# Performance work log

Hardware: AMD Instinct MI355X
Metric: run time of the kernel (lower is better)

## Reference

```python
import jax, jax.numpy as jnp
import numpy as np

B, T, N, D, K = 8, 64, 512, 64, 8
d = D // K  # per-head dim
NEG = -(2.0 ** 15) + 1.0  # -32767, as in source


def setup_inputs() -> dict:
    key = jax.random.key(0)
    ks = jax.random.split(key, 12)
    s = 0.05
    inp = {
        "x": jax.random.normal(ks[0], (B, T, N, D), dtype=jnp.float32),
        "ste": jax.random.normal(ks[1], (B, T, N, D), dtype=jnp.float32),
        "Wq": jax.random.normal(ks[2], (2 * D, D), dtype=jnp.float32) * s,
        "bq": jnp.zeros((D,), dtype=jnp.float32),
        "Wk": jax.random.normal(ks[3], (2 * D, D), dtype=jnp.float32) * s,
        "bk": jnp.zeros((D,), dtype=jnp.float32),
        "Wv": jax.random.normal(ks[4], (2 * D, D), dtype=jnp.float32) * s,
        "bv": jnp.zeros((D,), dtype=jnp.float32),
        "W1": jax.random.normal(ks[5], (D, D), dtype=jnp.float32) * s,
        "b1": jnp.zeros((D,), dtype=jnp.float32),
        "W2": jax.random.normal(ks[6], (D, D), dtype=jnp.float32) * s,
        "b2": jnp.zeros((D,), dtype=jnp.float32),
    }
    return inp


def reference(x, ste, Wq, bq, Wk, bk, Wv, bv, W1, b1, W2, b2):
    h = jnp.concatenate([x, ste], axis=-1)  # (B,T,N,2D)
    q = jax.nn.relu(jnp.einsum("btnf,fd->btnd", h, Wq) + bq)
    k = jax.nn.relu(jnp.einsum("btnf,fd->btnd", h, Wk) + bk)
    v = jax.nn.relu(jnp.einsum("btnf,fd->btnd", h, Wv) + bv)
    # split D into K heads of size d (torch split/cat over batch == head axis)
    q = q.reshape(B, T, N, K, d)
    k = k.reshape(B, T, N, K, d)
    v = v.reshape(B, T, N, K, d)
    scores = jnp.einsum("btnkd,bsnkd->bnkts", q, k) / jnp.sqrt(jnp.float32(d))
    causal = jnp.tril(jnp.ones((T, T), dtype=bool))  # (T,T)
    scores = jnp.where(causal, scores, jnp.float32(NEG))
    attn = jax.nn.softmax(scores, axis=-1)  # (B,N,K,T,T)
    out = jnp.einsum("bnkts,bsnkd->btnkd", attn, v).reshape(B, T, N, D)
    out = jax.nn.relu(jnp.einsum("btnd,de->btne", out, W1) + b1)
    out = jnp.einsum("btnd,de->btne", out, W2) + b2
    return out
```

## Files before the change

kernel.cpp:

```cpp
#include <hip/hip_runtime.h>


#define Bb 8
#define Tt 64
#define Nn 512
#define Dd 64

typedef unsigned short u16;
typedef unsigned int u32;
typedef __bf16 bf16x8 __attribute__((ext_vector_type(8)));
typedef float f32x4 __attribute__((ext_vector_type(4)));
typedef short s16x8 __attribute__((ext_vector_type(8)));

#define HS 136
#define QS 68

#define QSCALE 0.51006977f

#define WQ_OFF 0
#define WK_OFF 8192
#define WV_OFF 16384
#define W1_OFF 24576
#define W2_OFF 28672

__device__ inline u16 f2bf(float f) {
    u32 x = __float_as_uint(f);
    x += 0x7fffu + ((x >> 16) & 1u);
    return (u16)(x >> 16);
}
__device__ inline bf16x8 ldf(const u16* p) { return *(const bf16x8*)p; }
__device__ inline bf16x8 zf8() {
    s16x8 z = {0, 0, 0, 0, 0, 0, 0, 0};
    return __builtin_bit_cast(bf16x8, z);
}

__global__ __launch_bounds__(256)
void prep_weights(const float* __restrict__ Wq, const float* __restrict__ Wk,
                  const float* __restrict__ Wv, const float* __restrict__ W1,
                  const float* __restrict__ W2, u16* __restrict__ ws) {
    int t = blockIdx.x * 256 + threadIdx.x;
    if (t < 24576) {
        int m = t >> 13, r = t & 8191;
        const float* W = (m == 0) ? Wq : (m == 1) ? Wk : Wv;
        int f = r >> 6, c = r & 63;
        ws[m * 8192 + c * 128 + f] = f2bf(W[r]);
    } else {
        int t2 = t - 24576;
        int m = t2 >> 12, r = t2 & 4095;
        const float* W = m ? W2 : W1;
        int f = r >> 6, c = r & 63;
        ws[24576 + m * 4096 + c * 64 + f] = f2bf(W[r]);
    }
}

template<int MODE>
__device__ inline void mfma_gemm64(const u16* __restrict__ A, int As,
                                   const u16* __restrict__ Wg,
                                   const float* __restrict__ bias,
                                   u16* __restrict__ O, int Os,
                                   float* __restrict__ G,
                                   int w, int lane) {
    const int l15 = lane & 15, qd = lane >> 4;
    f32x4 acc[4];
#pragma unroll
    for (int ct = 0; ct < 4; ++ct) {
        float bv = bias[16 * ct + l15];
        acc[ct] = (f32x4){bv, bv, bv, bv};
    }
    const u16* arow = &A[(16 * w + l15) * As];
#pragma unroll
    for (int k0 = 0; k0 < 64; k0 += 32) {
        bf16x8 af = ldf(arow + k0 + qd * 8);
#pragma unroll
        for (int ct = 0; ct < 4; ++ct) {
            bf16x8 bfr = ldf(&Wg[(16 * ct + l15) * 64 + k0 + qd * 8]);
            acc[ct] = __builtin_amdgcn_mfma_f32_16x16x32_bf16(af, bfr, acc[ct], 0, 0, 0);
        }
    }
#pragma unroll
    for (int ct = 0; ct < 4; ++ct) {
        const int col = 16 * ct + l15;
#pragma unroll
        for (int r = 0; r < 4; ++r) {
            const int row = 16 * w + 4 * qd + r;
            float v = acc[ct][r];
            if (MODE == 0) { v = fmaxf(v, 0.f); O[row * Os + col] = f2bf(v); }
            else           { G[(size_t)row * (Nn * Dd) + col] = v; }
        }
    }
}

__global__ __launch_bounds__(256, 3)
void ta_fused_kernel(const float* __restrict__ x,  const float* __restrict__ ste,
                     const float* __restrict__ bq, const float* __restrict__ bk,
                     const float* __restrict__ bv_, const float* __restrict__ b1,
                     const float* __restrict__ b2, const u16* __restrict__ wsr,
                     float* __restrict__ out) {
    __shared__ __align__(16) u16 sm[21828];
    u16* h       = sm;
    u16* qb      = sm + 8704;
    u16* kb      = sm + 13056;
    u16* vT      = sm + 17408;
    u16* attnout = sm;
    u16* abuf    = qb;

    const int tid  = threadIdx.x;
    const int w    = tid >> 6;
    const int lane = tid & 63;
    const int l15  = lane & 15, qd = lane >> 4;
    const int bid  = blockIdx.x;
    const int b = bid >> 9, n = bid & 511;

    const float* xb = x   + (((size_t)b * Tt) * Nn + n) * Dd;
    const float* sb = ste + (((size_t)b * Tt) * Nn + n) * Dd;
    const u16* wq = wsr + WQ_OFF;
    const u16* wk = wsr + WK_OFF;
    const u16* wv = wsr + WV_OFF;

#pragma unroll
    for (int l = 0; l < 8; ++l) {
        int idx = l * 256 + tid;
        int t = idx >> 5, p = idx & 31;
        const float* src = (p < 16) ? xb : sb;
        float4 vv = *(const float4*)(src + (size_t)t * (Nn * Dd) + (p & 15) * 4);
        ushort4 st;
        st.x = f2bf(vv.x); st.y = f2bf(vv.y); st.z = f2bf(vv.z); st.w = f2bf(vv.w);
        *(ushort4*)&h[t * HS + p * 4] = st;
    }
    if (tid < 64) vT[64 * QS + tid] = 0x3F80;
    __syncthreads();

    {
        f32x4 qa[4], ka[4], va[4];
#pragma unroll
        for (int ct = 0; ct < 4; ++ct) {
            int c = 16 * ct + l15;
            float b0 = bq[c], b1v = bk[c], b2v = bv_[c];
            qa[ct] = (f32x4){b0, b0, b0, b0};
            ka[ct] = (f32x4){b1v, b1v, b1v, b1v};
            va[ct] = (f32x4){b2v, b2v, b2v, b2v};
        }
        const u16* arow = &h[(16 * w + l15) * HS];
#pragma unroll
        for (int k0 = 0; k0 < 128; k0 += 32) {
            bf16x8 af = ldf(arow + k0 + qd * 8);
#pragma unroll
            for (int ct = 0; ct < 4; ++ct) {
                const int boff = (16 * ct + l15) * 128 + k0 + qd * 8;
                bf16x8 bq8 = ldf(&wq[boff]);
                qa[ct] = __builtin_amdgcn_mfma_f32_16x16x32_bf16(af, bq8, qa[ct], 0, 0, 0);
                bf16x8 bk8 = ldf(&wk[boff]);
                ka[ct] = __builtin_amdgcn_mfma_f32_16x16x32_bf16(af, bk8, ka[ct], 0, 0, 0);
                bf16x8 bv8 = ldf(&wv[boff]);
                va[ct] = __builtin_amdgcn_mfma_f32_16x16x32_bf16(af, bv8, va[ct], 0, 0, 0);
            }
        }
#pragma unroll
        for (int ct = 0; ct < 4; ++ct) {
            const int col = 16 * ct + l15;
#pragma unroll
            for (int r = 0; r < 4; ++r) {
                const int row = 16 * w + 4 * qd + r;
                qb[row * QS + col] = f2bf(fmaxf(qa[ct][r], 0.f) * QSCALE);
                kb[row * QS + col] = f2bf(fmaxf(ka[ct][r], 0.f));
                vT[col * QS + row] = f2bf(fmaxf(va[ct][r], 0.f));
            }
        }
    }
    __syncthreads();

    u16* pb = sm + 4352 + 1088 * w;
    const bf16x8 z8 = zf8();
    const u16* qrow = &qb[(16 * w + l15) * QS];
#pragma unroll 1
    for (int h8 = 0; h8 < 64; h8 += 8) {
        bf16x8 af = (qd == 0) ? ldf(qrow + h8) : z8;
        f32x4 sv[4] = {{0,0,0,0},{0,0,0,0},{0,0,0,0},{0,0,0,0}};
#pragma unroll
        for (int ct = 0; ct < 4; ++ct) {
            bf16x8 bfr = (qd == 0) ? ldf(&kb[(16 * ct + l15) * QS + h8]) : z8;
            sv[ct] = __builtin_amdgcn_mfma_f32_16x16x32_bf16(af, bfr, sv[ct], 0, 0, 0);
        }
        const int tr = 16 * w + 4 * qd;
#pragma unroll
        for (int ct = 0; ct < 4; ++ct) {
            const int sc = 16 * ct + l15;
#pragma unroll
            for (int r = 0; r < 4; ++r)
                sv[ct][r] = (sc <= tr + r) ? exp2f(sv[ct][r]) : 0.f;
        }
#pragma unroll
        for (int ct = 0; ct < 4; ++ct)
#pragma unroll
            for (int r = 0; r < 4; ++r)
                pb[(4 * qd + r) * QS + 16 * ct + l15] = f2bf(sv[ct][r]);
        f32x4 o = {0, 0, 0, 0};
#pragma unroll
        for (int k0 = 0; k0 < 64; k0 += 32) {
            bf16x8 pa = ldf(&pb[l15 * QS + k0 + qd * 8]);
            const int vrow = (l15 < 8) ? (h8 + l15) : 64;
            bf16x8 vfr = (l15 <= 8) ? ldf(&vT[vrow * QS + k0 + qd * 8]) : z8;
            o = __builtin_amdgcn_mfma_f32_16x16x32_bf16(pa, vfr, o, 0, 0, 0);
        }
        const int dsrc = (lane & 48) | 8;
#pragma unroll
        for (int r = 0; r < 4; ++r) {
            float den = __shfl(o[r], dsrc, 64);
            if (l15 < 8)
                attnout[(16 * w + 4 * qd + r) * QS + h8 + l15] =
                    f2bf(o[r] * __builtin_amdgcn_rcpf(den));
        }
    }

    mfma_gemm64<0>(attnout, QS, wsr + W1_OFF, b1, abuf, QS, nullptr, w, lane);
    float* ob = out + (((size_t)b * Tt) * Nn + n) * Dd;
    mfma_gemm64<1>(abuf, QS, wsr + W2_OFF, b2, nullptr, 0, ob, w, lane);
}

extern "C" void kernel_launch(void* const* d_in, const int* in_sizes, int n_in,
                              void* d_out, int out_size, void* d_ws, size_t ws_size,
                              hipStream_t stream) {
    const float* x   = (const float*)d_in[0];
    const float* ste = (const float*)d_in[1];
    const float* Wq  = (const float*)d_in[2];
    const float* bq  = (const float*)d_in[3];
    const float* Wk  = (const float*)d_in[4];
    const float* bk  = (const float*)d_in[5];
    const float* Wv  = (const float*)d_in[6];
    const float* bv  = (const float*)d_in[7];
    const float* W1  = (const float*)d_in[8];
    const float* b1  = (const float*)d_in[9];
    const float* W2  = (const float*)d_in[10];
    const float* b2  = (const float*)d_in[11];
    float* out = (float*)d_out;
    u16* ws = (u16*)d_ws;

    hipLaunchKernelGGL(prep_weights, dim3(128), dim3(256), 0, stream,
                       Wq, Wk, Wv, W1, W2, ws);
    hipLaunchKernelGGL(ta_fused_kernel, dim3(Bb * Nn), dim3(256), 0, stream,
                       x, ste, bq, bk, bv, b1, b2, (const u16*)ws, out);
}
```

Before: 321.7 us.

## Hold weight fragments in registers, split GEMMs by output column, skip masked score tiles

Each wave now owns a 16-column slice of every projection and MLP output and loads its weight fragments into registers once, before the input staging. Before, every wave re-read all weight tiles from global memory for each GEMM. The attention loop also computes only the causal score tiles for the wave's row block, zero-fills the rest of the probability buffer once, and skips the second PV MFMA when it is not needed. This raises register pressure, adds block-wide barriers between the MLP stages that are needed now that waves exchange rows, and makes the loop trip counts differ per wave.

Result: faster. 313.7 us (-2.5%).

```diff
diff --git a/kernel.cpp b/kernel.cpp
--- a/kernel.cpp
+++ b/kernel.cpp
@@ -53,43 +53,6 @@
     }
 }
 
-template<int MODE>
-__device__ inline void mfma_gemm64(const u16* __restrict__ A, int As,
-                                   const u16* __restrict__ Wg,
-                                   const float* __restrict__ bias,
-                                   u16* __restrict__ O, int Os,
-                                   float* __restrict__ G,
-                                   int w, int lane) {
-    const int l15 = lane & 15, qd = lane >> 4;
-    f32x4 acc[4];
-#pragma unroll
-    for (int ct = 0; ct < 4; ++ct) {
-        float bv = bias[16 * ct + l15];
-        acc[ct] = (f32x4){bv, bv, bv, bv};
-    }
-    const u16* arow = &A[(16 * w + l15) * As];
-#pragma unroll
-    for (int k0 = 0; k0 < 64; k0 += 32) {
-        bf16x8 af = ldf(arow + k0 + qd * 8);
-#pragma unroll
-        for (int ct = 0; ct < 4; ++ct) {
-            bf16x8 bfr = ldf(&Wg[(16 * ct + l15) * 64 + k0 + qd * 8]);
-            acc[ct] = __builtin_amdgcn_mfma_f32_16x16x32_bf16(af, bfr, acc[ct], 0, 0, 0);
-        }
-    }
-#pragma unroll
-    for (int ct = 0; ct < 4; ++ct) {
-        const int col = 16 * ct + l15;
-#pragma unroll
-        for (int r = 0; r < 4; ++r) {
-            const int row = 16 * w + 4 * qd + r;
-            float v = acc[ct][r];
-            if (MODE == 0) { v = fmaxf(v, 0.f); O[row * Os + col] = f2bf(v); }
-            else           { G[(size_t)row * (Nn * Dd) + col] = v; }
-        }
-    }
-}
-
 __global__ __launch_bounds__(256, 3)
 void ta_fused_kernel(const float* __restrict__ x,  const float* __restrict__ ste,
                      const float* __restrict__ bq, const float* __restrict__ bk,
@@ -108,14 +71,31 @@
     const int w    = tid >> 6;
     const int lane = tid & 63;
     const int l15  = lane & 15, qd = lane >> 4;
+    const int wl   = 16 * w + l15;
     const int bid  = blockIdx.x;
     const int b = bid >> 9, n = bid & 511;
 
     const float* xb = x   + (((size_t)b * Tt) * Nn + n) * Dd;
     const float* sb = ste + (((size_t)b * Tt) * Nn + n) * Dd;
-    const u16* wq = wsr + WQ_OFF;
-    const u16* wk = wsr + WK_OFF;
-    const u16* wv = wsr + WV_OFF;
+
+    bf16x8 wqf[4], wkf[4], wvf[4], w1f[2], w2f[2];
+    {
+        const u16* pq = wsr + WQ_OFF + wl * 128 + qd * 8;
+        const u16* pk = wsr + WK_OFF + wl * 128 + qd * 8;
+        const u16* pv = wsr + WV_OFF + wl * 128 + qd * 8;
+#pragma unroll
+        for (int k0 = 0; k0 < 4; ++k0) {
+            wqf[k0] = ldf(pq + 32 * k0);
+            wkf[k0] = ldf(pk + 32 * k0);
+            wvf[k0] = ldf(pv + 32 * k0);
+        }
+        const u16* p1 = wsr + W1_OFF + wl * 64 + qd * 8;
+        const u16* p2 = wsr + W2_OFF + wl * 64 + qd * 8;
+        w1f[0] = ldf(p1); w1f[1] = ldf(p1 + 32);
+        w2f[0] = ldf(p2); w2f[1] = ldf(p2 + 32);
+    }
+    const float bqv = bq[wl], bkv = bk[wl], bvv = bv_[wl];
+    const float b1v = b1[wl], b2v = b2[wl];
 
 #pragma unroll
     for (int l = 0; l < 8; ++l) {
@@ -130,41 +110,25 @@
     if (tid < 64) vT[64 * QS + tid] = 0x3F80;
     __syncthreads();
 
-    {
-        f32x4 qa[4], ka[4], va[4];
-#pragma unroll
-        for (int ct = 0; ct < 4; ++ct) {
-            int c = 16 * ct + l15;
-            float b0 = bq[c], b1v = bk[c], b2v = bv_[c];
-            qa[ct] = (f32x4){b0, b0, b0, b0};
-            ka[ct] = (f32x4){b1v, b1v, b1v, b1v};
-            va[ct] = (f32x4){b2v, b2v, b2v, b2v};
-        }
-        const u16* arow = &h[(16 * w + l15) * HS];
-#pragma unroll
-        for (int k0 = 0; k0 < 128; k0 += 32) {
-            bf16x8 af = ldf(arow + k0 + qd * 8);
-#pragma unroll
-            for (int ct = 0; ct < 4; ++ct) {
-                const int boff = (16 * ct + l15) * 128 + k0 + qd * 8;
-                bf16x8 bq8 = ldf(&wq[boff]);
-                qa[ct] = __builtin_amdgcn_mfma_f32_16x16x32_bf16(af, bq8, qa[ct], 0, 0, 0);
-                bf16x8 bk8 = ldf(&wk[boff]);
-                ka[ct] = __builtin_amdgcn_mfma_f32_16x16x32_bf16(af, bk8, ka[ct], 0, 0, 0);
-                bf16x8 bv8 = ldf(&wv[boff]);
-                va[ct] = __builtin_amdgcn_mfma_f32_16x16x32_bf16(af, bv8, va[ct], 0, 0, 0);
-            }
-        }
-#pragma unroll
-        for (int ct = 0; ct < 4; ++ct) {
-            const int col = 16 * ct + l15;
-#pragma unroll
-            for (int r = 0; r < 4; ++r) {
-                const int row = 16 * w + 4 * qd + r;
-                qb[row * QS + col] = f2bf(fmaxf(qa[ct][r], 0.f) * QSCALE);
-                kb[row * QS + col] = f2bf(fmaxf(ka[ct][r], 0.f));
-                vT[col * QS + row] = f2bf(fmaxf(va[ct][r], 0.f));
-            }
+#pragma unroll
+    for (int rt = 0; rt < 4; ++rt) {
+        f32x4 qa = {bqv, bqv, bqv, bqv};
+        f32x4 ka = {bkv, bkv, bkv, bkv};
+        f32x4 va = {bvv, bvv, bvv, bvv};
+        const u16* arow = &h[(16 * rt + l15) * HS + qd * 8];
+#pragma unroll
+        for (int k0 = 0; k0 < 4; ++k0) {
+            bf16x8 af = ldf(arow + 32 * k0);
+            qa = __builtin_amdgcn_mfma_f32_16x16x32_bf16(af, wqf[k0], qa, 0, 0, 0);
+            ka = __builtin_amdgcn_mfma_f32_16x16x32_bf16(af, wkf[k0], ka, 0, 0, 0);
+            va = __builtin_amdgcn_mfma_f32_16x16x32_bf16(af, wvf[k0], va, 0, 0, 0);
+        }
+#pragma unroll
+        for (int r = 0; r < 4; ++r) {
+            const int row = 16 * rt + 4 * qd + r;
+            qb[row * QS + wl] = f2bf(fmaxf(qa[r], 0.f) * QSCALE);
+            kb[row * QS + wl] = f2bf(fmaxf(ka[r], 0.f));
+            vT[wl * QS + row] = f2bf(fmaxf(va[r], 0.f));
         }
     }
     __syncthreads();
@@ -172,35 +136,45 @@
     u16* pb = sm + 4352 + 1088 * w;
     const bf16x8 z8 = zf8();
     const u16* qrow = &qb[(16 * w + l15) * QS];
+    const int nct = w + 1;
+    for (int ct = nct; ct < 4; ++ct)
+#pragma unroll
+        for (int r = 0; r < 4; ++r)
+            pb[(4 * qd + r) * QS + 16 * ct + l15] = 0;
+
 #pragma unroll 1
     for (int h8 = 0; h8 < 64; h8 += 8) {
         bf16x8 af = (qd == 0) ? ldf(qrow + h8) : z8;
-        f32x4 sv[4] = {{0,0,0,0},{0,0,0,0},{0,0,0,0},{0,0,0,0}};
-#pragma unroll
-        for (int ct = 0; ct < 4; ++ct) {
+        f32x4 sv[4];
+        for (int ct = 0; ct < nct; ++ct) {
+            f32x4 zz = {0, 0, 0, 0};
             bf16x8 bfr = (qd == 0) ? ldf(&kb[(16 * ct + l15) * QS + h8]) : z8;
-            sv[ct] = __builtin_amdgcn_mfma_f32_16x16x32_bf16(af, bfr, sv[ct], 0, 0, 0);
+            sv[ct] = __builtin_amdgcn_mfma_f32_16x16x32_bf16(af, bfr, zz, 0, 0, 0);
         }
         const int tr = 16 * w + 4 * qd;
-#pragma unroll
-        for (int ct = 0; ct < 4; ++ct) {
+        for (int ct = 0; ct < nct; ++ct) {
             const int sc = 16 * ct + l15;
 #pragma unroll
             for (int r = 0; r < 4; ++r)
                 sv[ct][r] = (sc <= tr + r) ? exp2f(sv[ct][r]) : 0.f;
         }
-#pragma unroll
-        for (int ct = 0; ct < 4; ++ct)
+        for (int ct = 0; ct < nct; ++ct)
 #pragma unroll
             for (int r = 0; r < 4; ++r)
                 pb[(4 * qd + r) * QS + 16 * ct + l15] = f2bf(sv[ct][r]);
         f32x4 o = {0, 0, 0, 0};
-#pragma unroll
-        for (int k0 = 0; k0 < 64; k0 += 32) {
-            bf16x8 pa = ldf(&pb[l15 * QS + k0 + qd * 8]);
+        {
             const int vrow = (l15 < 8) ? (h8 + l15) : 64;
-            bf16x8 vfr = (l15 <= 8) ? ldf(&vT[vrow * QS + k0 + qd * 8]) : z8;
+            bf16x8 pa = ldf(&pb[l15 * QS + qd * 8]);
+            bf16x8 vfr = ldf(&vT[vrow * QS + qd * 8]);
+            if (l15 > 8) vfr = z8;
             o = __builtin_amdgcn_mfma_f32_16x16x32_bf16(pa, vfr, o, 0, 0, 0);
+            if (nct > 2) {
+                bf16x8 pa2 = ldf(&pb[l15 * QS + 32 + qd * 8]);
+                bf16x8 vfr2 = ldf(&vT[vrow * QS + 32 + qd * 8]);
+                if (l15 > 8) vfr2 = z8;
+                o = __builtin_amdgcn_mfma_f32_16x16x32_bf16(pa2, vfr2, o, 0, 0, 0);
+            }
         }
         const int dsrc = (lane & 48) | 8;
 #pragma unroll
@@ -211,10 +185,30 @@
                     f2bf(o[r] * __builtin_amdgcn_rcpf(den));
         }
     }
-
-    mfma_gemm64<0>(attnout, QS, wsr + W1_OFF, b1, abuf, QS, nullptr, w, lane);
+    __syncthreads();
+
+#pragma unroll
+    for (int rt = 0; rt < 4; ++rt) {
+        f32x4 a1 = {b1v, b1v, b1v, b1v};
+        const u16* arow = &attnout[(16 * rt + l15) * QS + qd * 8];
+        a1 = __builtin_amdgcn_mfma_f32_16x16x32_bf16(ldf(arow), w1f[0], a1, 0, 0, 0);
+        a1 = __builtin_amdgcn_mfma_f32_16x16x32_bf16(ldf(arow + 32), w1f[1], a1, 0, 0, 0);
+#pragma unroll
+        for (int r = 0; r < 4; ++r)
+            abuf[(16 * rt + 4 * qd + r) * QS + wl] = f2bf(fmaxf(a1[r], 0.f));
+    }
+    __syncthreads();
     float* ob = out + (((size_t)b * Tt) * Nn + n) * Dd;
-    mfma_gemm64<1>(abuf, QS, wsr + W2_OFF, b2, nullptr, 0, ob, w, lane);
+#pragma unroll
+    for (int rt = 0; rt < 4; ++rt) {
+        f32x4 a2 = {b2v, b2v, b2v, b2v};
+        const u16* arow = &abuf[(16 * rt + l15) * QS + qd * 8];
+        a2 = __builtin_amdgcn_mfma_f32_16x16x32_bf16(ldf(arow), w2f[0], a2, 0, 0, 0);
+        a2 = __builtin_amdgcn_mfma_f32_16x16x32_bf16(ldf(arow + 32), w2f[1], a2, 0, 0, 0);
+#pragma unroll
+        for (int r = 0; r < 4; ++r)
+            ob[(size_t)(16 * rt + 4 * qd + r) * (Nn * Dd) + wl] = a2[r];
+    }
 }
 
 extern "C" void kernel_launch(void* const* d_in, const int* in_sizes, int n_in,
```
